# Optimization experiments

Measured on AMD Instinct MI355X. Metric: run time of the kernel, lower is better.

The kernel has to match this reference:

```python
import jax, jax.numpy as jnp
import numpy as np

B, DIN, F, H, C = 8192, 2048, 2048, 2048, 345
EPS = 1e-5


def setup_inputs() -> dict:
    key = jax.random.key(0)
    ks = jax.random.split(key, 8)
    rng = np.random.default_rng(0)
    # labels and sort order (torch.sort is stable here via argsort kind='stable')
    y_np = rng.integers(0, C, size=B).astype(np.int64)
    order_np = np.argsort(y_np, kind='stable')
    ys = y_np[order_np]
    # per-class random permutations within each sorted segment (torch.randperm per interval)
    shuf1 = np.empty(B, dtype=np.int64)
    shuf2 = np.empty(B, dtype=np.int64)
    for c in np.unique(ys):
        idx = np.nonzero(ys == c)[0]
        shuf1[idx] = rng.permutation(idx)
        shuf2[idx] = rng.permutation(idx)
    s = 0.02  # weight init scale
    return {
        'x': jax.random.normal(ks[0], (B, DIN), jnp.float32),
        'lam': jnp.array([float(rng.beta(0.5, 0.5))], jnp.float32),
        'Wf': jax.random.normal(ks[1], (DIN, F), jnp.float32) * s,
        'bf': jnp.zeros((F,), jnp.float32),
        'W1': jax.random.normal(ks[2], (F, H), jnp.float32) * s,
        'b1': jnp.zeros((H,), jnp.float32),
        'g1': jnp.ones((H,), jnp.float32),
        'be1': jnp.zeros((H,), jnp.float32),
        'W2': jax.random.normal(ks[3], (H, H), jnp.float32) * s,
        'b2': jnp.zeros((H,), jnp.float32),
        'g2': jnp.ones((H,), jnp.float32),
        'be2': jnp.zeros((H,), jnp.float32),
        'W3': jax.random.normal(ks[4], (H, F), jnp.float32) * s,
        'b3': jnp.zeros((F,), jnp.float32),
        'g3': jnp.ones((F,), jnp.float32),
        'be3': jnp.zeros((F,), jnp.float32),
        'Wc': jax.random.normal(ks[5], (F, C), jnp.float32) * s,
        'bc': jnp.zeros((C,), jnp.float32),
        'y': jnp.asarray(y_np),
        'order': jnp.asarray(order_np),
        'shuf1': jnp.asarray(shuf1),
        'shuf2': jnp.asarray(shuf2),
    }


def _bn(x, g, b):
    # BatchNorm1d, training mode: biased batch stats
    m = jnp.mean(x, axis=0)
    v = jnp.var(x, axis=0)
    return (x - m) * jax.lax.rsqrt(v + EPS) * g + b


def reference(x, lam, Wf, bf, W1, b1, g1, be1, W2, b2, g2, be2, W3, b3, g3, be3, Wc, bc, y, order, shuf1, shuf2):
    lam = lam[0]
    xs = x[order]           # sorted-by-label gather (vectorized)
    ys = y[order]
    feat = jax.nn.relu(xs @ Wf + bf)                      # featurizer
    h = jax.nn.relu(_bn(feat @ W1 + b1, g1, be1))         # cdpl projector
    h = jax.nn.relu(_bn(h @ W2 + b2, g2, be2))
    proj = _bn(h @ W3 + b3, g3, be3)
    out = feat @ Wc + bc                                  # classifier logits
    out2, feat2 = out[shuf1], proj[shuf1]                 # per-class shuffles
    out3, feat3 = out[shuf2], proj[shuf2]
    out3 = lam * out2 + (1.0 - lam) * out3
    feat3 = lam * feat2 + (1.0 - lam) * feat3
    mse = lambda a, b: jnp.mean((a - b) ** 2)
    L_ind_logit = mse(out, out2)
    L_hdl_logit = mse(out, out3)
    L_ind_feat = 0.3 * mse(proj, feat2)
    L_hdl_feat = 0.3 * mse(proj, feat3)
    logp = jax.nn.log_softmax(out, axis=-1)
    cl_loss = -jnp.mean(jnp.take_along_axis(logp, ys[:, None], axis=-1))
    C_scale = jax.lax.stop_gradient(jnp.minimum(cl_loss, 1.0))  # .item() -> constant
    loss = cl_loss + C_scale * (lam * (L_ind_logit + L_ind_feat) + (1.0 - lam) * (L_hdl_logit + L_hdl_feat))
    return loss
```

## Files before the change

### kernel.cpp

```cpp
#include <hip/hip_runtime.h>

#define NB   8192
#define NF   2048
#define NC   345
#define NCP  384
#define EPSV 1e-5f

#define SX   (5.75f / 127.0f)
#define SW   (0.115f / 127.0f)
#define SF   (5.2f / 127.0f)
#define SH   (5.75f / 127.0f)
#define ST1  (3.34f / 127.0f)
#define ST2  (3.68f / 127.0f)
#define QX   (1.0f / SX)
#define QW   (1.0f / SW)
#define QF   (1.0f / SF)
#define QH   (1.0f / SH)
#define QT1  (1.0f / ST1)
#define QT2  (1.0f / ST2)

typedef __bf16 bf16x8 __attribute__((ext_vector_type(8)));
typedef float  f32x4  __attribute__((ext_vector_type(4)));
typedef int    i32x4  __attribute__((ext_vector_type(4)));

__device__ __forceinline__ float bs2f(unsigned int u) { return __uint_as_float(u << 16); }
__device__ __forceinline__ unsigned short f2bs(float f) {
    unsigned int u = __float_as_uint(f);
    u += 0x7fffu + ((u >> 16) & 1u);
    return (unsigned short)(u >> 16);
}
__device__ __forceinline__ int q8i(float v, float iq) {
    int t = __float2int_rn(v * iq);
    return t > 127 ? 127 : (t < -127 ? -127 : t);
}

#define GLD16(g, l)                                                                     \
    __builtin_amdgcn_global_load_lds((const __attribute__((address_space(1))) void*)(g),\
                                     (__attribute__((address_space(3))) void*)(l),      \
                                     16, 0, 0)

__global__ void k_gather(const float* __restrict__ x, const int* __restrict__ order,
                         char* __restrict__ xq) {
    const int row = blockIdx.x;
    const long src = order[row];
    const float4* xr = (const float4*)(x + src * 2048);
    float4 a = xr[threadIdx.x * 2 + 0];
    float4 b = xr[threadIdx.x * 2 + 1];
    unsigned int lo = (unsigned)(q8i(a.x, QX) & 255) | ((unsigned)(q8i(a.y, QX) & 255) << 8) |
                      ((unsigned)(q8i(a.z, QX) & 255) << 16) | ((unsigned)(q8i(a.w, QX) & 255) << 24);
    unsigned int hi = (unsigned)(q8i(b.x, QX) & 255) | ((unsigned)(q8i(b.y, QX) & 255) << 8) |
                      ((unsigned)(q8i(b.z, QX) & 255) << 16) | ((unsigned)(q8i(b.w, QX) & 255) << 24);
    uint2 o; o.x = lo; o.y = hi;
    ((uint2*)(xq + (long)row * 2048))[threadIdx.x] = o;
}

template <int Q8>
__global__ void k_transpose(const float* __restrict__ W, char* __restrict__ Wt8,
                            unsigned short* __restrict__ Wtb, int K, int N, int Npad) {
    __shared__ float tile[32][33];
    const int n0 = blockIdx.x * 32, k0 = blockIdx.y * 32;
    const int tx = threadIdx.x, ty = threadIdx.y;
    #pragma unroll
    for (int i = 0; i < 32; i += 8) {
        int n = n0 + tx, k = k0 + ty + i;
        tile[ty + i][tx] = (n < N) ? W[(long)k * N + n] : 0.f;
    }
    __syncthreads();
    #pragma unroll
    for (int i = 0; i < 32; i += 8) {
        int n = n0 + ty + i, k = k0 + tx;
        if (n < Npad) {
            if (Q8) Wt8[(long)n * K + k] = (char)q8i(tile[tx][ty + i], QW);
            else    Wtb[(long)n * K + k] = f2bs(tile[tx][ty + i]);
        }
    }
}

__global__ void k_padbias(const float* __restrict__ bc, float* __restrict__ bcp) {
    const int i = threadIdx.x + blockIdx.x * blockDim.x;
    if (i < NCP) bcp[i] = (i < NC) ? bc[i] : 0.f;
}

#define BARX  do { asm volatile("" ::: "memory"); __builtin_amdgcn_s_barrier(); \
                   asm volatile("" ::: "memory"); } while (0)
#define LGKM0 asm volatile("s_waitcnt lgkmcnt(0)" ::: "memory")
#define VMW4  asm volatile("s_waitcnt vmcnt(4)" ::: "memory")
#define VMW0  asm volatile("s_waitcnt vmcnt(0)" ::: "memory")

#define RDX(u, AV, BV) do {                                                            \
    const char* A_ = &L[((u) & 3) * 32768];                                            \
    const char* B_ = A_ + 16384;                                                       \
    _Pragma("unroll") for (int m_ = 0; m_ < 8; m_++)                                   \
        AV[m_] = *(const i32x4*)&A_[(wm * 128 + m_ * 16 + frow) * 64 + slt];           \
    _Pragma("unroll") for (int n_ = 0; n_ < 4; n_++)                                   \
        BV[n_] = *(const i32x4*)&B_[(wn * 64 + n_ * 16 + frow) * 64 + slt];            \
} while (0)

#define MMX(AV, BV) do {                                                               \
    __builtin_amdgcn_s_setprio(1);                                                     \
    _Pragma("unroll") for (int n_ = 0; n_ < 4; n_++)                                   \
    _Pragma("unroll") for (int m_ = 0; m_ < 8; m_++)                                   \
        acc[m_][n_] = __builtin_amdgcn_mfma_i32_16x16x64_i8(BV[n_], AV[m_],            \
                                                            acc[m_][n_], 0, 0, 0);    \
    __builtin_amdgcn_s_setprio(0);                                                     \
} while (0)

template <int RELU, int STATS, int B16OUT, int I8OUT>
__global__ __launch_bounds__(512, 2) void k_gemmq(
    const char* __restrict__ A,
    const char* __restrict__ Bt,
    const float* __restrict__ bias,
    unsigned short* __restrict__ Cb,
    char* __restrict__ C8,
    float* __restrict__ stats,
    float S, float IQ, int N, int K) {
    __shared__ char L[4 * 32768];
    const int tid  = threadIdx.x;
    const int lane = tid & 63;
    const int wv   = tid >> 6;
    const int frow = lane & 15;
    const int kg   = lane >> 4;
    const int wm   = wv >> 2;
    const int wn   = wv & 3;
    const int slt  = (kg ^ ((frow >> 1) & 3)) * 16;

    const int id  = blockIdx.x;
    const int xcd = id & 7, kid = id >> 3;
    const int brow = (xcd * 4 + (kid & 3)) * 256;
    const int bcol = (kid >> 2) * 256;

    const char* pA[2];
    const char* pB[2];
    #pragma unroll
    for (int i = 0; i < 2; i++) {
        const int q = tid + i * 512;
        const int j = q >> 2;
        const int c = (q & 3) ^ ((j >> 1) & 3);
        pA[i] = A  + (long)(brow + j) * K + c * 16;
        pB[i] = Bt + (long)(bcol + j) * K + c * 16;
    }

    i32x4 acc[8][4];
    #pragma unroll
    for (int m = 0; m < 8; m++)
        #pragma unroll
        for (int n = 0; n < 4; n++)
            #pragma unroll
            for (int r = 0; r < 4; r++) acc[m][n][r] = 0;

    auto stage = [&](int s) {
        char* Lb = &L[(s & 3) * 32768];
        const int ko = s * 64;
        GLD16(pA[0] + ko, Lb + wv * 1024);
        GLD16(pA[1] + ko, Lb + 8192 + wv * 1024);
        GLD16(pB[0] + ko, Lb + 16384 + wv * 1024);
        GLD16(pB[1] + ko, Lb + 24576 + wv * 1024);
    };

    i32x4 avA[8], bvA[4], avB[8], bvB[4];

    stage(0); stage(1); stage(2);
    VMW4; BARX;
    RDX(0, avA, bvA);

    for (int i = 0; i < 14; i++) {
        const int t = i * 2;
        RDX(t + 1, avB, bvB); stage(t + 3); MMX(avA, bvA); VMW4; BARX;
        RDX(t + 2, avA, bvA); stage(t + 4); MMX(avB, bvB); VMW4; BARX;
    }
    RDX(29, avB, bvB); stage(31); MMX(avA, bvA); VMW4; BARX;
    RDX(30, avA, bvA); MMX(avB, bvB); VMW0; BARX;
    RDX(31, avB, bvB); MMX(avA, bvA);
    MMX(avB, bvB);

    LGKM0; BARX;
    unsigned short* Ls = (unsigned short*)L;
    const int cbase = bcol + wn * 64 + kg * 4;
    #pragma unroll
    for (int n = 0; n < 4; n++) {
        const int col = cbase + n * 16;
        const float4 bb = *(const float4*)&bias[col];
        float s0_ = 0.f, s1_ = 0.f, s2_ = 0.f, s3_ = 0.f;
        float q0_ = 0.f, q1_ = 0.f, q2_ = 0.f, q3_ = 0.f;
        const int s8 = wn * 16 + n * 4 + kg;
        const int p8 = s8 ^ frow;
        #pragma unroll
        for (int m = 0; m < 8; m++) {
            const int rloc = wm * 128 + m * 16 + frow;
            float v0 = (float)acc[m][n][0] * S + bb.x;
            float v1 = (float)acc[m][n][1] * S + bb.y;
            float v2 = (float)acc[m][n][2] * S + bb.z;
            float v3 = (float)acc[m][n][3] * S + bb.w;
            if (STATS) { s0_ += v0; q0_ += v0 * v0; s1_ += v1; q1_ += v1 * v1;
                         s2_ += v2; q2_ += v2 * v2; s3_ += v3; q3_ += v3 * v3; }
            if (RELU) { v0 = fmaxf(v0, 0.f); v1 = fmaxf(v1, 0.f);
                        v2 = fmaxf(v2, 0.f); v3 = fmaxf(v3, 0.f); }
            ushort4 st; st.x = f2bs(v0); st.y = f2bs(v1); st.z = f2bs(v2); st.w = f2bs(v3);
            *(ushort4*)&Ls[rloc * 256 + p8 * 4] = st;
        }
        if (STATS) {
            #pragma unroll
            for (int off = 1; off <= 8; off <<= 1) {
                s0_ += __shfl_xor(s0_, off); s1_ += __shfl_xor(s1_, off);
                s2_ += __shfl_xor(s2_, off); s3_ += __shfl_xor(s3_, off);
                q0_ += __shfl_xor(q0_, off); q1_ += __shfl_xor(q1_, off);
                q2_ += __shfl_xor(q2_, off); q3_ += __shfl_xor(q3_, off);
            }
            if (frow == 0) {
                atomicAdd(&stats[col + 0], s0_); atomicAdd(&stats[col + 1], s1_);
                atomicAdd(&stats[col + 2], s2_); atomicAdd(&stats[col + 3], s3_);
                atomicAdd(&stats[N + col + 0], q0_); atomicAdd(&stats[N + col + 1], q1_);
                atomicAdd(&stats[N + col + 2], q2_); atomicAdd(&stats[N + col + 3], q3_);
            }
        }
    }
    LGKM0; BARX;
    #pragma unroll
    for (int it = 0; it < 16; it++) {
        const int c  = tid + it * 512;
        const int r  = c >> 5;
        const int a  = c & 31;
        const int x  = r & 15;
        const int a2 = a ^ (x >> 1);
        uint4 v = *(const uint4*)&Ls[r * 256 + a2 * 8];
        if (x & 1) { unsigned tx_ = v.x, ty_ = v.y; v.x = v.z; v.y = v.w; v.z = tx_; v.w = ty_; }
        const long grow = brow + r;
        const int  gcol = bcol + a * 8;
        if (B16OUT) *(uint4*)&Cb[grow * N + gcol] = v;
        if (I8OUT) {
            unsigned int us[8] = {v.x & 0xffffu, v.x >> 16, v.y & 0xffffu, v.y >> 16,
                                  v.z & 0xffffu, v.z >> 16, v.w & 0xffffu, v.w >> 16};
            unsigned int b[8];
            #pragma unroll
            for (int j = 0; j < 8; j++) b[j] = (unsigned)(q8i(bs2f(us[j]), IQ) & 255);
            uint2 o;
            o.x = b[0] | (b[1] << 8) | (b[2] << 16) | (b[3] << 24);
            o.y = b[4] | (b[5] << 8) | (b[6] << 16) | (b[7] << 24);
            *(uint2*)&C8[grow * N + gcol] = o;
        }
    }
}

__global__ __launch_bounds__(256) void k_gemm(const unsigned short* __restrict__ A,
                                              const unsigned short* __restrict__ Bt,
                                              const float* __restrict__ bias,
                                              float* __restrict__ Cf,
                                              int M, int N, int K, int ldc) {
    constexpr int BK = 64;
    __shared__ unsigned short As[128 * BK];
    __shared__ unsigned short Bs[128 * BK];
    const int tid  = threadIdx.x;
    const int lane = tid & 63;
    const int wv   = tid >> 6;
    const int brow = blockIdx.x * 128;
    const int bcol = blockIdx.y * 128;
    const int wr   = (wv >> 1) * 64;
    const int wc   = (wv & 1) * 64;
    const int frow = lane & 15;
    const int kg   = lane >> 4;
    const int rx   = frow & 7;
    const int srow  = lane >> 3;
    const int sslot = (lane & 7) ^ srow;

    f32x4 acc[4][4];
    #pragma unroll
    for (int m = 0; m < 4; m++)
        #pragma unroll
        for (int n = 0; n < 4; n++)
            #pragma unroll
            for (int r = 0; r < 4; r++) acc[m][n][r] = 0.f;

    for (int kt = 0; kt < K; kt += BK) {
        #pragma unroll
        for (int i = 0; i < 4; i++) {
            const int c = wv * 4 + i;
            const int r = c * 8 + srow;
            GLD16(A + (long)(brow + r) * K + kt + sslot * 8, &As[c * 512]);
        }
        #pragma unroll
        for (int i = 0; i < 4; i++) {
            const int c = wv * 4 + i;
            const int r = c * 8 + srow;
            GLD16(Bt + (long)(bcol + r) * K + kt + sslot * 8, &Bs[c * 512]);
        }
        __syncthreads();
        #pragma unroll
        for (int kk = 0; kk < 2; kk++) {
            bf16x8 av[4], bv[4];
            #pragma unroll
            for (int m = 0; m < 4; m++) {
                const int row = wr + m * 16 + frow;
                av[m] = *(const bf16x8*)&As[row * BK + (((kk * 4 + kg) ^ rx) * 8)];
            }
            #pragma unroll
            for (int n = 0; n < 4; n++) {
                const int row = wc + n * 16 + frow;
                bv[n] = *(const bf16x8*)&Bs[row * BK + (((kk * 4 + kg) ^ rx) * 8)];
            }
            #pragma unroll
            for (int m = 0; m < 4; m++)
                #pragma unroll
                for (int n = 0; n < 4; n++)
                    acc[m][n] = __builtin_amdgcn_mfma_f32_16x16x32_bf16(bv[n], av[m],
                                                                        acc[m][n], 0, 0, 0);
        }
        __syncthreads();
    }
    const int r0 = brow + wr + frow;
    const int c0 = bcol + wc + kg * 4;
    #pragma unroll
    for (int n = 0; n < 4; n++) {
        const int col = c0 + n * 16;
        const float4 bb = *(const float4*)&bias[col];
        #pragma unroll
        for (int m = 0; m < 4; m++) {
            const long row = r0 + m * 16;
            float4 o;
            o.x = acc[m][n][0] + bb.x; o.y = acc[m][n][1] + bb.y;
            o.z = acc[m][n][2] + bb.z; o.w = acc[m][n][3] + bb.w;
            *(float4*)&Cf[row * ldc + col] = o;
        }
    }
}

__global__ void k_bnfin(float* __restrict__ sums, const float* __restrict__ g,
                        const float* __restrict__ be, int ncols) {
    const int c = blockIdx.x * blockDim.x + threadIdx.x;
    const float m   = sums[c] * (1.f / NB);
    const float var = sums[ncols + c] * (1.f / NB) - m * m;
    const float sc  = rsqrtf(var + EPSV) * g[c];
    sums[c] = sc;
    sums[ncols + c] = be[c] - m * sc;
}

__global__ void k_bnapplyq8(const char* __restrict__ t8, const float* __restrict__ sums,
                            char* __restrict__ o8, float St, int ncols) {
    const long i  = ((long)blockIdx.x * blockDim.x + threadIdx.x) * 8;
    const int  c0 = (int)(i & (ncols - 1));
    uint2 v = *(const uint2*)(t8 + i);
    unsigned int b[8];
    #pragma unroll
    for (int j = 0; j < 8; j++) {
        const unsigned int w = (j < 4) ? v.x : v.y;
        const int raw = (int)(signed char)((w >> ((j & 3) * 8)) & 0xffu);
        const int c = c0 + j;
        float val = (float)raw * St * sums[c] + sums[ncols + c];
        val = fmaxf(val, 0.f);
        b[j] = (unsigned)(q8i(val, QH) & 255);
    }
    uint2 o;
    o.x = b[0] | (b[1] << 8) | (b[2] << 16) | (b[3] << 24);
    o.y = b[4] | (b[5] << 8) | (b[6] << 16) | (b[7] << 24);
    *(uint2*)(o8 + i) = o;
}

__global__ __launch_bounds__(256) void k_logitloss(const float* __restrict__ out,
                            const int* __restrict__ y,
                            const int* __restrict__ order, const int* __restrict__ s1,
                            const int* __restrict__ s2, const float* __restrict__ lamp,
                            float* __restrict__ acc) {
    const int lane = threadIdx.x & 63;
    const int wv   = threadIdx.x >> 6;
    const int wid  = blockIdx.x * 4 + wv;
    const int nw   = gridDim.x * 4;
    const float lam = lamp[0];
    float ce = 0.f, d1 = 0.f, d2 = 0.f;
    for (int i = wid; i < NB; i += nw) {
        const float* o  = out + (long)i * NCP;
        const float* o2 = out + (long)s1[i] * NCP;
        const float* o3 = out + (long)s2[i] * NCP;
        float v[6];
        float mx = -1e30f;
        #pragma unroll
        for (int j = 0; j < 6; j++) {
            const int c = lane + j * 64;
            if (c < NC) {
                const float a = o[c], b = o2[c], cc = o3[c];
                const float mix = lam * b + (1.f - lam) * cc;
                v[j] = a;
                d1 += (a - b) * (a - b);
                d2 += (a - mix) * (a - mix);
                mx = fmaxf(mx, a);
            } else v[j] = -1e30f;
        }
        #pragma unroll
        for (int off = 32; off; off >>= 1) mx = fmaxf(mx, __shfl_xor(mx, off));
        float se = 0.f;
        #pragma unroll
        for (int j = 0; j < 6; j++) se += expf(v[j] - mx);
        #pragma unroll
        for (int off = 32; off; off >>= 1) se += __shfl_xor(se, off);
        if (lane == 0) {
            const int yv = y[order[i]];
            ce += mx + logf(se) - o[yv];
        }
    }
    #pragma unroll
    for (int off = 32; off; off >>= 1) {
        d1 += __shfl_xor(d1, off);
        d2 += __shfl_xor(d2, off);
    }
    __shared__ float red[4][3];
    if (lane == 0) { red[wv][0] = ce; red[wv][1] = d1; red[wv][2] = d2; }
    __syncthreads();
    if (threadIdx.x == 0) {
        atomicAdd(&acc[0], red[0][0] + red[1][0] + red[2][0] + red[3][0]);
        atomicAdd(&acc[1], red[0][1] + red[1][1] + red[2][1] + red[3][1]);
        atomicAdd(&acc[2], red[0][2] + red[1][2] + red[2][2] + red[3][2]);
    }
}

__global__ __launch_bounds__(256) void k_featloss(const unsigned short* __restrict__ t3,
                           const float* __restrict__ st,
                           const int* __restrict__ s1,
                           const int* __restrict__ s2, const float* __restrict__ lamp,
                           float* __restrict__ acc) {
    const int t = threadIdx.x;
    const float lam = lamp[0];
    float sc[8], sh[8];
    #pragma unroll
    for (int j = 0; j < 8; j++) { sc[j] = st[t * 8 + j]; sh[j] = st[NF + t * 8 + j]; }
    float d1 = 0.f, d2 = 0.f;
    for (int i = blockIdx.x; i < NB; i += gridDim.x) {
        uint4 a = ((const uint4*)(t3 + (long)i * NF))[t];
        uint4 b = ((const uint4*)(t3 + (long)s1[i] * NF))[t];
        uint4 c = ((const uint4*)(t3 + (long)s2[i] * NF))[t];
        unsigned int ua[8] = {a.x & 0xffffu, a.x >> 16, a.y & 0xffffu, a.y >> 16,
                              a.z & 0xffffu, a.z >> 16, a.w & 0xffffu, a.w >> 16};
        unsigned int ub[8] = {b.x & 0xffffu, b.x >> 16, b.y & 0xffffu, b.y >> 16,
                              b.z & 0xffffu, b.z >> 16, b.w & 0xffffu, b.w >> 16};
        unsigned int uc[8] = {c.x & 0xffffu, c.x >> 16, c.y & 0xffffu, c.y >> 16,
                              c.z & 0xffffu, c.z >> 16, c.w & 0xffffu, c.w >> 16};
        #pragma unroll
        for (int j = 0; j < 8; j++) {
            float pa = sc[j] * bs2f(ua[j]) + sh[j];
            float pb = sc[j] * bs2f(ub[j]) + sh[j];
            float pc = sc[j] * bs2f(uc[j]) + sh[j];
            float mix = lam * pb + (1.f - lam) * pc;
            d1 += (pa - pb) * (pa - pb);
            d2 += (pa - mix) * (pa - mix);
        }
    }
    #pragma unroll
    for (int off = 32; off; off >>= 1) {
        d1 += __shfl_xor(d1, off);
        d2 += __shfl_xor(d2, off);
    }
    __shared__ float r1[4], r2[4];
    if ((t & 63) == 0) { r1[t >> 6] = d1; r2[t >> 6] = d2; }
    __syncthreads();
    if (t == 0) {
        atomicAdd(&acc[3], r1[0] + r1[1] + r1[2] + r1[3]);
        atomicAdd(&acc[4], r2[0] + r2[1] + r2[2] + r2[3]);
    }
}

__global__ void k_final(const float* __restrict__ acc, const float* __restrict__ lamp,
                        float* __restrict__ outp) {
    const float lam = lamp[0];
    const float cl  = acc[0] * (1.f / NB);
    const float Lil = acc[1] * (1.f / ((float)NB * NC));
    const float Lhl = acc[2] * (1.f / ((float)NB * NC));
    const float Lif = 0.3f * acc[3] * (1.f / ((float)NB * NF));
    const float Lhf = 0.3f * acc[4] * (1.f / ((float)NB * NF));
    const float Cs  = fminf(cl, 1.f);
    outp[0] = cl + Cs * (lam * (Lil + Lif) + (1.f - lam) * (Lhl + Lhf));
}

extern "C" void kernel_launch(void* const* d_in, const int* in_sizes, int n_in,
                              void* d_out, int out_size, void* d_ws, size_t ws_size,
                              hipStream_t stream) {
    const float* x   = (const float*)d_in[0];
    const float* lam = (const float*)d_in[1];
    const float* Wf  = (const float*)d_in[2];
    const float* bf_ = (const float*)d_in[3];
    const float* W1  = (const float*)d_in[4];
    const float* b1  = (const float*)d_in[5];
    const float* g1  = (const float*)d_in[6];
    const float* be1 = (const float*)d_in[7];
    const float* W2  = (const float*)d_in[8];
    const float* b2  = (const float*)d_in[9];
    const float* g2  = (const float*)d_in[10];
    const float* be2 = (const float*)d_in[11];
    const float* W3  = (const float*)d_in[12];
    const float* b3  = (const float*)d_in[13];
    const float* g3  = (const float*)d_in[14];
    const float* be3 = (const float*)d_in[15];
    const float* Wc  = (const float*)d_in[16];
    const float* bc  = (const float*)d_in[17];
    const int* y     = (const int*)d_in[18];
    const int* order = (const int*)d_in[19];
    const int* s1    = (const int*)d_in[20];
    const int* s2    = (const int*)d_in[21];
    float* outp = (float*)d_out;

    char* ws = (char*)d_ws;
    const size_t MB = 1024 * 1024;
    char*           R0  = ws;
    char*           R1  = ws + 16 * MB;
    unsigned short* R1b = (unsigned short*)R1;
    char*           R2  = ws + 48 * MB;
    char*           R3  = ws + 64 * MB;
    float*          outbuf = (float*)(ws + 80 * MB);
    char*           WT0 = ws + 92 * MB;
    char*           WT1 = ws + 96 * MB;
    char*           WT2 = ws + 100 * MB;
    char*           WT3 = ws + 104 * MB;
    unsigned short* WCT = (unsigned short*)(ws + 108 * MB);
    float* stats = (float*)(ws + 110 * MB);
    float* accs  = stats + 3 * 4096;
    float* bcp   = accs + 16;

    hipMemsetAsync(stats, 0, (3 * 4096 + 8) * sizeof(float), stream);

    dim3 tb(32, 8);
    k_transpose<1><<<dim3(64, 64), tb, 0, stream>>>(Wf, WT0, nullptr, 2048, 2048, 2048);
    k_transpose<1><<<dim3(64, 64), tb, 0, stream>>>(W1, WT1, nullptr, 2048, 2048, 2048);
    k_transpose<1><<<dim3(64, 64), tb, 0, stream>>>(W2, WT2, nullptr, 2048, 2048, 2048);
    k_transpose<1><<<dim3(64, 64), tb, 0, stream>>>(W3, WT3, nullptr, 2048, 2048, 2048);
    k_transpose<0><<<dim3(12, 64), tb, 0, stream>>>(Wc, nullptr, WCT, 2048, NC, NCP);
    k_padbias<<<2, 192, 0, stream>>>(bc, bcp);

    k_gather<<<NB, 256, 0, stream>>>(x, order, R0);

    k_gemmq<1, 0, 1, 1><<<256, 512, 0, stream>>>(R0, WT0, bf_, R1b, R2, nullptr,
                                                 SX * SW, QF, 2048, 2048);
    k_gemm<<<dim3(64, 3), 256, 0, stream>>>(R1b, WCT, bcp, outbuf, NB, NC, 2048, NCP);
    k_gemmq<0, 1, 0, 1><<<256, 512, 0, stream>>>(R2, WT1, b1, nullptr, R3, stats,
                                                 SF * SW, QT1, 2048, 2048);
    k_bnfin<<<8, 256, 0, stream>>>(stats, g1, be1, 2048);
    k_bnapplyq8<<<8192, 256, 0, stream>>>(R3, stats, R0, ST1, 2048);
    k_gemmq<0, 1, 0, 1><<<256, 512, 0, stream>>>(R0, WT2, b2, nullptr, R3, stats + 4096,
                                                 SH * SW, QT2, 2048, 2048);
    k_bnfin<<<8, 256, 0, stream>>>(stats + 4096, g2, be2, 2048);
    k_bnapplyq8<<<8192, 256, 0, stream>>>(R3, stats + 4096, R2, ST2, 2048);
    k_gemmq<0, 1, 1, 0><<<256, 512, 0, stream>>>(R2, WT3, b3, R1b, nullptr, stats + 8192,
                                                 SH * SW, 0.f, 2048, 2048);
    k_bnfin<<<8, 256, 0, stream>>>(stats + 8192, g3, be3, 2048);

    k_logitloss<<<512, 256, 0, stream>>>(outbuf, y, order, s1, s2, lam, accs);
    k_featloss<<<512, 256, 0, stream>>>(R1b, stats + 8192, s1, s2, lam, accs);
    k_final<<<1, 1, 0, stream>>>(accs, lam, outp);
}
```

Measured before the change: 325.5 us.

## Move classifier GEMM and final projection output to int8, fuse BN finalize

The classifier GEMM now reads the int8-quantized featurizer output and uses int8 MFMA instead of bf16. The last projector GEMM writes int8 instead of bf16, which halves feature-loss gather traffic. The BN finalize kernels are folded into the apply and loss kernels, and the four weight transposes are merged into one launch. Together these cut memory traffic and launch count. The cost is extra quantization error in the logits and projection features, which could shift the loss.

```diff
diff --git a/kernel.cpp b/kernel.cpp
--- a/kernel.cpp
+++ b/kernel.cpp
@@ -54,9 +54,26 @@
     ((uint2*)(xq + (long)row * 2048))[threadIdx.x] = o;
 }
 
-template <int Q8>
-__global__ void k_transpose(const float* __restrict__ W, char* __restrict__ Wt8,
-                            unsigned short* __restrict__ Wtb, int K, int N, int Npad) {
+__global__ void k_transpose4(const float* __restrict__ W0, const float* __restrict__ W1,
+                             const float* __restrict__ W2, const float* __restrict__ W3,
+                             char* __restrict__ Wt) {
+    __shared__ float tile[32][33];
+    const float* Wz = (blockIdx.z == 0) ? W0 : (blockIdx.z == 1) ? W1
+                     : (blockIdx.z == 2) ? W2 : W3;
+    char* out = Wt + (size_t)blockIdx.z * 2048 * 2048;
+    const int n0 = blockIdx.x * 32, k0 = blockIdx.y * 32;
+    const int tx = threadIdx.x, ty = threadIdx.y;
+    #pragma unroll
+    for (int i = 0; i < 32; i += 8)
+        tile[ty + i][tx] = Wz[(long)(k0 + ty + i) * 2048 + n0 + tx];
+    __syncthreads();
+    #pragma unroll
+    for (int i = 0; i < 32; i += 8)
+        out[(long)(n0 + ty + i) * 2048 + k0 + tx] = (char)q8i(tile[tx][ty + i], QW);
+}
+
+__global__ void k_transposeC(const float* __restrict__ W, char* __restrict__ Wt8,
+                             int K, int N, int Npad) {
     __shared__ float tile[32][33];
     const int n0 = blockIdx.x * 32, k0 = blockIdx.y * 32;
     const int tx = threadIdx.x, ty = threadIdx.y;
@@ -69,10 +86,7 @@
     #pragma unroll
     for (int i = 0; i < 32; i += 8) {
         int n = n0 + ty + i, k = k0 + tx;
-        if (n < Npad) {
-            if (Q8) Wt8[(long)n * K + k] = (char)q8i(tile[tx][ty + i], QW);
-            else    Wtb[(long)n * K + k] = f2bs(tile[tx][ty + i]);
-        }
+        if (n < Npad) Wt8[(long)n * K + k] = (char)q8i(tile[tx][ty + i], QW);
     }
 }
 
@@ -105,12 +119,11 @@
     __builtin_amdgcn_s_setprio(0);                                                     \
 } while (0)
 
-template <int RELU, int STATS, int B16OUT, int I8OUT>
+template <int RELU, int STATS>
 __global__ __launch_bounds__(512, 2) void k_gemmq(
     const char* __restrict__ A,
     const char* __restrict__ Bt,
     const float* __restrict__ bias,
-    unsigned short* __restrict__ Cb,
     char* __restrict__ C8,
     float* __restrict__ stats,
     float S, float IQ, int N, int K) {
@@ -226,29 +239,25 @@
         if (x & 1) { unsigned tx_ = v.x, ty_ = v.y; v.x = v.z; v.y = v.w; v.z = tx_; v.w = ty_; }
         const long grow = brow + r;
         const int  gcol = bcol + a * 8;
-        if (B16OUT) *(uint4*)&Cb[grow * N + gcol] = v;
-        if (I8OUT) {
-            unsigned int us[8] = {v.x & 0xffffu, v.x >> 16, v.y & 0xffffu, v.y >> 16,
-                                  v.z & 0xffffu, v.z >> 16, v.w & 0xffffu, v.w >> 16};
-            unsigned int b[8];
-            #pragma unroll
-            for (int j = 0; j < 8; j++) b[j] = (unsigned)(q8i(bs2f(us[j]), IQ) & 255);
-            uint2 o;
-            o.x = b[0] | (b[1] << 8) | (b[2] << 16) | (b[3] << 24);
-            o.y = b[4] | (b[5] << 8) | (b[6] << 16) | (b[7] << 24);
-            *(uint2*)&C8[grow * N + gcol] = o;
-        }
-    }
-}
-
-__global__ __launch_bounds__(256) void k_gemm(const unsigned short* __restrict__ A,
-                                              const unsigned short* __restrict__ Bt,
-                                              const float* __restrict__ bias,
-                                              float* __restrict__ Cf,
-                                              int M, int N, int K, int ldc) {
-    constexpr int BK = 64;
-    __shared__ unsigned short As[128 * BK];
-    __shared__ unsigned short Bs[128 * BK];
+        unsigned int us[8] = {v.x & 0xffffu, v.x >> 16, v.y & 0xffffu, v.y >> 16,
+                              v.z & 0xffffu, v.z >> 16, v.w & 0xffffu, v.w >> 16};
+        unsigned int b[8];
+        #pragma unroll
+        for (int j = 0; j < 8; j++) b[j] = (unsigned)(q8i(bs2f(us[j]), IQ) & 255);
+        uint2 o;
+        o.x = b[0] | (b[1] << 8) | (b[2] << 16) | (b[3] << 24);
+        o.y = b[4] | (b[5] << 8) | (b[6] << 16) | (b[7] << 24);
+        *(uint2*)&C8[grow * N + gcol] = o;
+    }
+}
+
+__global__ __launch_bounds__(256) void k_gemmc(const char* __restrict__ A,
+                                               const char* __restrict__ Bt,
+                                               const float* __restrict__ bias,
+                                               float* __restrict__ Cf,
+                                               float S, int K, int ldc) {
+    __shared__ char As[8192];
+    __shared__ char Bs[8192];
     const int tid  = threadIdx.x;
     const int lane = tid & 63;
     const int wv   = tid >> 6;
@@ -258,52 +267,46 @@
     const int wc   = (wv & 1) * 64;
     const int frow = lane & 15;
     const int kg   = lane >> 4;
-    const int rx   = frow & 7;
-    const int srow  = lane >> 3;
-    const int sslot = (lane & 7) ^ srow;
-
-    f32x4 acc[4][4];
+    const int slt  = (kg ^ ((frow >> 1) & 3)) * 16;
+
+    const char* pA[2];
+    const char* pB[2];
+    #pragma unroll
+    for (int i = 0; i < 2; i++) {
+        const int q = tid + i * 256;
+        const int j = q >> 2;
+        const int c = (q & 3) ^ ((j >> 1) & 3);
+        pA[i] = A  + (long)(brow + j) * K + c * 16;
+        pB[i] = Bt + (long)(bcol + j) * K + c * 16;
+    }
+
+    i32x4 acc[4][4];
     #pragma unroll
     for (int m = 0; m < 4; m++)
         #pragma unroll
         for (int n = 0; n < 4; n++)
             #pragma unroll
-            for (int r = 0; r < 4; r++) acc[m][n][r] = 0.f;
-
-    for (int kt = 0; kt < K; kt += BK) {
-        #pragma unroll
-        for (int i = 0; i < 4; i++) {
-            const int c = wv * 4 + i;
-            const int r = c * 8 + srow;
-            GLD16(A + (long)(brow + r) * K + kt + sslot * 8, &As[c * 512]);
-        }
-        #pragma unroll
-        for (int i = 0; i < 4; i++) {
-            const int c = wv * 4 + i;
-            const int r = c * 8 + srow;
-            GLD16(Bt + (long)(bcol + r) * K + kt + sslot * 8, &Bs[c * 512]);
-        }
+            for (int r = 0; r < 4; r++) acc[m][n][r] = 0;
+
+    for (int kt = 0; kt < K; kt += 64) {
+        GLD16(pA[0] + kt, As + wv * 1024);
+        GLD16(pA[1] + kt, As + 4096 + wv * 1024);
+        GLD16(pB[0] + kt, Bs + wv * 1024);
+        GLD16(pB[1] + kt, Bs + 4096 + wv * 1024);
         __syncthreads();
-        #pragma unroll
-        for (int kk = 0; kk < 2; kk++) {
-            bf16x8 av[4], bv[4];
+        i32x4 av[4], bv[4];
+        #pragma unroll
+        for (int m = 0; m < 4; m++)
+            av[m] = *(const i32x4*)&As[(wr + m * 16 + frow) * 64 + slt];
+        #pragma unroll
+        for (int n = 0; n < 4; n++)
+            bv[n] = *(const i32x4*)&Bs[(wc + n * 16 + frow) * 64 + slt];
+        #pragma unroll
+        for (int m = 0; m < 4; m++)
             #pragma unroll
-            for (int m = 0; m < 4; m++) {
-                const int row = wr + m * 16 + frow;
-                av[m] = *(const bf16x8*)&As[row * BK + (((kk * 4 + kg) ^ rx) * 8)];
-            }
-            #pragma unroll
-            for (int n = 0; n < 4; n++) {
-                const int row = wc + n * 16 + frow;
-                bv[n] = *(const bf16x8*)&Bs[row * BK + (((kk * 4 + kg) ^ rx) * 8)];
-            }
-            #pragma unroll
-            for (int m = 0; m < 4; m++)
-                #pragma unroll
-                for (int n = 0; n < 4; n++)
-                    acc[m][n] = __builtin_amdgcn_mfma_f32_16x16x32_bf16(bv[n], av[m],
-                                                                        acc[m][n], 0, 0, 0);
-        }
+            for (int n = 0; n < 4; n++)
+                acc[m][n] = __builtin_amdgcn_mfma_i32_16x16x64_i8(bv[n], av[m],
+                                                                  acc[m][n], 0, 0, 0);
         __syncthreads();
     }
     const int r0 = brow + wr + frow;
@@ -316,35 +319,37 @@
         for (int m = 0; m < 4; m++) {
             const long row = r0 + m * 16;
             float4 o;
-            o.x = acc[m][n][0] + bb.x; o.y = acc[m][n][1] + bb.y;
-            o.z = acc[m][n][2] + bb.z; o.w = acc[m][n][3] + bb.w;
+            o.x = (float)acc[m][n][0] * S + bb.x;
+            o.y = (float)acc[m][n][1] * S + bb.y;
+            o.z = (float)acc[m][n][2] * S + bb.z;
+            o.w = (float)acc[m][n][3] * S + bb.w;
             *(float4*)&Cf[row * ldc + col] = o;
         }
     }
 }
 
-__global__ void k_bnfin(float* __restrict__ sums, const float* __restrict__ g,
-                        const float* __restrict__ be, int ncols) {
-    const int c = blockIdx.x * blockDim.x + threadIdx.x;
-    const float m   = sums[c] * (1.f / NB);
-    const float var = sums[ncols + c] * (1.f / NB) - m * m;
-    const float sc  = rsqrtf(var + EPSV) * g[c];
-    sums[c] = sc;
-    sums[ncols + c] = be[c] - m * sc;
-}
-
 __global__ void k_bnapplyq8(const char* __restrict__ t8, const float* __restrict__ sums,
+                            const float* __restrict__ g, const float* __restrict__ be,
                             char* __restrict__ o8, float St, int ncols) {
     const long i  = ((long)blockIdx.x * blockDim.x + threadIdx.x) * 8;
     const int  c0 = (int)(i & (ncols - 1));
+    float sc[8], sh[8];
+    #pragma unroll
+    for (int j = 0; j < 8; j++) {
+        const int c = c0 + j;
+        const float m   = sums[c] * (1.f / NB);
+        const float var = sums[ncols + c] * (1.f / NB) - m * m;
+        const float s   = rsqrtf(var + EPSV) * g[c];
+        sc[j] = s * St;
+        sh[j] = be[c] - m * s;
+    }
     uint2 v = *(const uint2*)(t8 + i);
     unsigned int b[8];
     #pragma unroll
     for (int j = 0; j < 8; j++) {
         const unsigned int w = (j < 4) ? v.x : v.y;
         const int raw = (int)(signed char)((w >> ((j & 3) * 8)) & 0xffu);
-        const int c = c0 + j;
-        float val = (float)raw * St * sums[c] + sums[ncols + c];
+        float val = (float)raw * sc[j] + sh[j];
         val = fmaxf(val, 0.f);
         b[j] = (unsigned)(q8i(val, QH) & 255);
     }
@@ -410,8 +415,9 @@
     }
 }
 
-__global__ __launch_bounds__(256) void k_featloss(const unsigned short* __restrict__ t3,
-                           const float* __restrict__ st,
+__global__ __launch_bounds__(256) void k_featloss(const char* __restrict__ t3q,
+                           const float* __restrict__ sums,
+                           const float* __restrict__ g, const float* __restrict__ be,
                            const int* __restrict__ s1,
                            const int* __restrict__ s2, const float* __restrict__ lamp,
                            float* __restrict__ acc) {
@@ -419,23 +425,28 @@
     const float lam = lamp[0];
     float sc[8], sh[8];
     #pragma unroll
-    for (int j = 0; j < 8; j++) { sc[j] = st[t * 8 + j]; sh[j] = st[NF + t * 8 + j]; }
+    for (int j = 0; j < 8; j++) {
+        const int c = t * 8 + j;
+        const float m   = sums[c] * (1.f / NB);
+        const float var = sums[NF + c] * (1.f / NB) - m * m;
+        const float s   = rsqrtf(var + EPSV) * g[c];
+        sc[j] = s * ST2;
+        sh[j] = be[c] - m * s;
+    }
     float d1 = 0.f, d2 = 0.f;
     for (int i = blockIdx.x; i < NB; i += gridDim.x) {
-        uint4 a = ((const uint4*)(t3 + (long)i * NF))[t];
-        uint4 b = ((const uint4*)(t3 + (long)s1[i] * NF))[t];
-        uint4 c = ((const uint4*)(t3 + (long)s2[i] * NF))[t];
-        unsigned int ua[8] = {a.x & 0xffffu, a.x >> 16, a.y & 0xffffu, a.y >> 16,
-                              a.z & 0xffffu, a.z >> 16, a.w & 0xffffu, a.w >> 16};
-        unsigned int ub[8] = {b.x & 0xffffu, b.x >> 16, b.y & 0xffffu, b.y >> 16,
-                              b.z & 0xffffu, b.z >> 16, b.w & 0xffffu, b.w >> 16};
-        unsigned int uc[8] = {c.x & 0xffffu, c.x >> 16, c.y & 0xffffu, c.y >> 16,
-                              c.z & 0xffffu, c.z >> 16, c.w & 0xffffu, c.w >> 16};
+        uint2 a = ((const uint2*)(t3q + (long)i * NF))[t];
+        uint2 b = ((const uint2*)(t3q + (long)s1[i] * NF))[t];
+        uint2 c = ((const uint2*)(t3q + (long)s2[i] * NF))[t];
         #pragma unroll
         for (int j = 0; j < 8; j++) {
-            float pa = sc[j] * bs2f(ua[j]) + sh[j];
-            float pb = sc[j] * bs2f(ub[j]) + sh[j];
-            float pc = sc[j] * bs2f(uc[j]) + sh[j];
+            const unsigned int wa = (j < 4) ? a.x : a.y;
+            const unsigned int wb = (j < 4) ? b.x : b.y;
+            const unsigned int wc_ = (j < 4) ? c.x : c.y;
+            const int sh8 = (j & 3) * 8;
+            float pa = (float)(int)(signed char)((wa >> sh8) & 0xffu) * sc[j] + sh[j];
+            float pb = (float)(int)(signed char)((wb >> sh8) & 0xffu) * sc[j] + sh[j];
+            float pc = (float)(int)(signed char)((wc_ >> sh8) & 0xffu) * sc[j] + sh[j];
             float mix = lam * pb + (1.f - lam) * pc;
             d1 += (pa - pb) * (pa - pb);
             d2 += (pa - mix) * (pa - mix);
@@ -496,49 +507,38 @@
 
     char* ws = (char*)d_ws;
     const size_t MB = 1024 * 1024;
-    char*           R0  = ws;
-    char*           R1  = ws + 16 * MB;
-    unsigned short* R1b = (unsigned short*)R1;
-    char*           R2  = ws + 48 * MB;
-    char*           R3  = ws + 64 * MB;
-    float*          outbuf = (float*)(ws + 80 * MB);
-    char*           WT0 = ws + 92 * MB;
-    char*           WT1 = ws + 96 * MB;
-    char*           WT2 = ws + 100 * MB;
-    char*           WT3 = ws + 104 * MB;
-    unsigned short* WCT = (unsigned short*)(ws + 108 * MB);
-    float* stats = (float*)(ws + 110 * MB);
+    char*  R0  = ws;
+    char*  R2  = ws + 16 * MB;
+    char*  R3  = ws + 32 * MB;
+    float* outbuf = (float*)(ws + 48 * MB);
+    char*  WT  = ws + 60 * MB;
+    char*  WCT8 = ws + 76 * MB;
+    float* stats = (float*)(ws + 77 * MB);
     float* accs  = stats + 3 * 4096;
     float* bcp   = accs + 16;
 
     hipMemsetAsync(stats, 0, (3 * 4096 + 8) * sizeof(float), stream);
 
     dim3 tb(32, 8);
-    k_transpose<1><<<dim3(64, 64), tb, 0, stream>>>(Wf, WT0, nullptr, 2048, 2048, 2048);
-    k_transpose<1><<<dim3(64, 64), tb, 0, stream>>>(W1, WT1, nullptr, 2048, 2048, 2048);
-    k_transpose<1><<<dim3(64, 64), tb, 0, stream>>>(W2, WT2, nullptr, 2048, 2048, 2048);
-    k_transpose<1><<<dim3(64, 64), tb, 0, stream>>>(W3, WT3, nullptr, 2048, 2048, 2048);
-    k_transpose<0><<<dim3(12, 64), tb, 0, stream>>>(Wc, nullptr, WCT, 2048, NC, NCP);
+    k_transpose4<<<dim3(64, 64, 4), tb, 0, stream>>>(Wf, W1, W2, W3, WT);
+    k_transposeC<<<dim3(12, 64), tb, 0, stream>>>(Wc, WCT8, 2048, NC, NCP);
     k_padbias<<<2, 192, 0, stream>>>(bc, bcp);
 
     k_gather<<<NB, 256, 0, stream>>>(x, order, R0);
 
-    k_gemmq<1, 0, 1, 1><<<256, 512, 0, stream>>>(R0, WT0, bf_, R1b, R2, nullptr,
-                                                 SX * SW, QF, 2048, 2048);
-    k_gemm<<<dim3(64, 3), 256, 0, stream>>>(R1b, WCT, bcp, outbuf, NB, NC, 2048, NCP);
-    k_gemmq<0, 1, 0, 1><<<256, 512, 0, stream>>>(R2, WT1, b1, nullptr, R3, stats,
-                                                 SF * SW, QT1, 2048, 2048);
-    k_bnfin<<<8, 256, 0, stream>>>(stats, g1, be1, 2048);
-    k_bnapplyq8<<<8192, 256, 0, stream>>>(R3, stats, R0, ST1, 2048);
-    k_gemmq<0, 1, 0, 1><<<256, 512, 0, stream>>>(R0, WT2, b2, nullptr, R3, stats + 4096,
-                                                 SH * SW, QT2, 2048, 2048);
-    k_bnfin<<<8, 256, 0, stream>>>(stats + 4096, g2, be2, 2048);
-    k_bnapplyq8<<<8192, 256, 0, stream>>>(R3, stats + 4096, R2, ST2, 2048);
-    k_gemmq<0, 1, 1, 0><<<256, 512, 0, stream>>>(R2, WT3, b3, R1b, nullptr, stats + 8192,
-                                                 SH * SW, 0.f, 2048, 2048);
-    k_bnfin<<<8, 256, 0, stream>>>(stats + 8192, g3, be3, 2048);
+    k_gemmq<1, 0><<<256, 512, 0, stream>>>(R0, WT, bf_, R2, nullptr,
+                                           SX * SW, QF, 2048, 2048);
+    k_gemmc<<<dim3(64, 3), 256, 0, stream>>>(R2, WCT8, bcp, outbuf, SF * SW, 2048, NCP);
+    k_gemmq<0, 1><<<256, 512, 0, stream>>>(R2, WT + 4 * MB, b1, R3, stats,
+                                           SF * SW, QT1, 2048, 2048);
+    k_bnapplyq8<<<8192, 256, 0, stream>>>(R3, stats, g1, be1, R0, ST1, 2048);
+    k_gemmq<0, 1><<<256, 512, 0, stream>>>(R0, WT + 8 * MB, b2, R3, stats + 4096,
+                                           SH * SW, QT2, 2048, 2048);
+    k_bnapplyq8<<<8192, 256, 0, stream>>>(R3, stats + 4096, g2, be2, R2, ST2, 2048);
+    k_gemmq<0, 1><<<256, 512, 0, stream>>>(R2, WT + 12 * MB, b3, R3, stats + 8192,
+                                           SH * SW, QT2, 2048, 2048);
 
     k_logitloss<<<512, 256, 0, stream>>>(outbuf, y, order, s1, s2, lam, accs);
-    k_featloss<<<512, 256, 0, stream>>>(R1b, stats + 8192, s1, s2, lam, accs);
+    k_featloss<<<512, 256, 0, stream>>>(R3, stats + 8192, g3, be3, s1, s2, lam, accs);
     k_final<<<1, 1, 0, stream>>>(accs, lam, outp);
 }
```

Result: faster. 308.4 us (-5.3%).
